# Kernel optimization log

Hardware: AMD Instinct MI355X
Metric: run time of the kernel (lower is better)

Reference implementation:

```python
import jax, jax.numpy as jnp
import numpy as np
from jax import lax

B, FREQ, T = 4, 258, 2176
N_FRAMES, N_SHIFT = 128, 64
W = 32            # number of spectral windows: 128 + 64*k < 2176
H = 5 * 28 * 14   # 1960
NUM_CLASSES = 2


def setup_inputs() -> dict:
    key = jax.random.key(0)
    ks = jax.random.split(key, 13)
    x = jax.random.normal(ks[0], (B, FREQ, T), jnp.float32)
    hx0 = jax.random.normal(ks[1], (B, H), jnp.float32)
    labels = jax.random.randint(ks[2], (B,), 0, NUM_CLASSES, jnp.int64)
    conv1_w = jax.random.normal(ks[3], (64, 1, 9, 9), jnp.float32) * 0.05
    conv1_b = jax.random.normal(ks[4], (64,), jnp.float32) * 0.05
    conv2_w = jax.random.normal(ks[5], (5, 64, 4, 4), jnp.float32) * 0.05
    conv2_b = jax.random.normal(ks[6], (5,), jnp.float32) * 0.05
    w_ih = jax.random.normal(ks[7], (3 * H, H), jnp.float32) * 0.02
    w_hh = jax.random.normal(ks[8], (3 * H, H), jnp.float32) * 0.02
    b_ih = jax.random.normal(ks[9], (3 * H,), jnp.float32) * 0.02
    b_hh = jax.random.normal(ks[10], (3 * H,), jnp.float32) * 0.02
    fc_w = jax.random.normal(ks[11], (NUM_CLASSES, H), jnp.float32) * 0.02
    fc_b = jax.random.normal(ks[12], (NUM_CLASSES,), jnp.float32) * 0.02
    return dict(x=x, hx0=hx0, labels=labels, conv1_w=conv1_w, conv1_b=conv1_b,
                conv2_w=conv2_w, conv2_b=conv2_b, w_ih=w_ih, w_hh=w_hh,
                b_ih=b_ih, b_hh=b_hh, fc_w=fc_w, fc_b=fc_b)


def _conv_sig_pool(y, w, b, pad):
    y = lax.conv_general_dilated(y, w, (1, 1), [(pad, pad), (pad, pad)],
                                 dimension_numbers=('NCHW', 'OIHW', 'NCHW'))
    y = jax.nn.sigmoid(y + b[None, :, None, None])
    return lax.reduce_window(y, -jnp.inf, lax.max, (1, 1, 3, 3), (1, 1, 3, 3), 'VALID')


def reference(x, hx0, labels, conv1_w, conv1_b, conv2_w, conv2_b,
              w_ih, w_hh, b_ih, b_hh, fc_w, fc_b):
    # spectral windows: drop first freq bin, slide window of 128 frames, stride 64
    loc = x[:, 1:, :]                                   # [B, 257, T]
    idx = jnp.arange(W)[:, None] * N_SHIFT + jnp.arange(N_FRAMES)[None, :]
    win = loc[:, :, idx]                                # [B, 257, W, 128]
    win = win.transpose(0, 2, 1, 3).reshape(B * W, 1, 257, N_FRAMES)

    y = _conv_sig_pool(win, conv1_w, conv1_b, 2)        # [B*W, 64, 84, 41]
    y = _conv_sig_pool(y, conv2_w, conv2_b, 2)          # [B*W, 5, 28, 14]
    feat = y.reshape(B, W, H)                           # flatten C,H,W (C-order)

    def gru_step(h, xt):                                # xt: [B, H]
        gi = xt @ w_ih.T + b_ih                         # [B, 3H]
        gh = h @ w_hh.T + b_hh
        i_r, i_z, i_n = jnp.split(gi, 3, axis=1)
        h_r, h_z, h_n = jnp.split(gh, 3, axis=1)
        r = jax.nn.sigmoid(i_r + h_r)
        z = jax.nn.sigmoid(i_z + h_z)
        n = jnp.tanh(i_n + r * h_n)
        return (1.0 - z) * n + z * h, None

    hT, _ = lax.scan(gru_step, hx0, feat.transpose(1, 0, 2))  # scan over W steps

    logits = hT @ fc_w.T + fc_b                         # [B, num_classes]
    samples = jax.nn.softmax(logits, axis=1)
    return (samples, labels)
```

## Files before the change

kernel.cpp:

```cpp
#include <hip/hip_runtime.h>
#include <hip/hip_cooperative_groups.h>

__device__ __forceinline__ float bf2f(unsigned short u) {
  union { unsigned int i; float f; } v; v.i = ((unsigned int)u) << 16; return v.f;
}
__device__ __forceinline__ unsigned short f2bf(float f) {
  union { float f; unsigned int i; } v; v.f = f;
  unsigned int x = v.i;
  return (unsigned short)((x + 0x7fffu + ((x >> 16) & 1u)) >> 16);
}
__device__ __forceinline__ float sigmf(float x) { return 1.f / (1.f + __expf(-x)); }

typedef float f32x4 __attribute__((ext_vector_type(4)));
typedef short short8v __attribute__((ext_vector_type(8)));
typedef short short4v __attribute__((ext_vector_type(4)));

__device__ __forceinline__ short8v pack8(const float* p) {
  union { short8v s; unsigned int u[4]; } r;
#pragma unroll
  for (int i = 0; i < 4; ++i) {
    unsigned int lo = __float_as_uint(p[2 * i]) >> 16;
    unsigned int hi = __float_as_uint(p[2 * i + 1]) & 0xFFFF0000u;
    r.u[i] = hi | lo;
  }
  return r.s;
}

#define KP 1984
#define NP 5888
#define GRU_BLOCKS 245
#define C1_PLANE 2860

__global__ void k_prep(const float* __restrict__ w_hh, unsigned short* __restrict__ whh_bf,
                       const float* __restrict__ w_ih, unsigned short* __restrict__ wih_bf,
                       const float* __restrict__ w1, const float* __restrict__ b1,
                       unsigned short* __restrict__ w1f,
                       const float* __restrict__ w2, unsigned short* __restrict__ w2f,
                       unsigned short* __restrict__ feat_bf,
                       unsigned long long* __restrict__ hb0,
                       unsigned long long* __restrict__ hb1) {
  const int b = blockIdx.x;
  const int tid = threadIdx.x;
  if (b < 2048) {
    const int n4 = 5880 * 1960 / 4;
    for (int i = b * 256 + tid; i < n4; i += 2048 * 256) {
      float4 v = *reinterpret_cast<const float4*>(&w_hh[i * 4]);
      ushort4 u;
      u.x = f2bf(v.x); u.y = f2bf(v.y); u.z = f2bf(v.z); u.w = f2bf(v.w);
      *reinterpret_cast<ushort4*>(&whh_bf[i * 4]) = u;
    }
  } else if (b < 7752) {
    const int total = NP * KP / 8;
    int idx = (b - 2048) * 256 + tid;
    if (idx < total) {
      int row = idx / (KP / 8);
      int c8 = (idx - row * (KP / 8)) * 8;
      short8v v = {0, 0, 0, 0, 0, 0, 0, 0};
      if (row < 5880 && c8 < 1960) {
        const float* s = w_ih + (size_t)row * 1960 + c8;
        if (c8 + 8 <= 1960) {
          float tmp[8];
#pragma unroll
          for (int i = 0; i < 8; ++i) tmp[i] = s[i];
          v = pack8(tmp);
        } else {
          union { short8v s8; unsigned short us[8]; } u; u.s8 = v;
          for (int i = 0; i < 1960 - c8; ++i) u.us[i] = f2bf(s[i]);
          v = u.s8;
        }
      }
      *reinterpret_cast<short8v*>(wih_bf + (size_t)idx * 8) = v;
    }
  } else if (b < 7776) {
    int idx = (b - 7752) * 256 + tid;
    if (idx < 4 * 3 * 64 * 8) {
      int j = idx & 7, l = (idx >> 3) & 63;
      int rest = idx >> 9;
      int s = rest % 3, ocf = rest / 3;
      int oc = ocf * 16 + (l & 15);
      int k = s * 32 + (l >> 4) * 8 + j;
      float v = 0.f;
      if (k < 64)       v = w1[oc * 81 + (k >> 3) * 9 + (k & 7)];
      else if (k < 72)  v = w1[oc * 81 + 72 + (k - 64)];
      else if (k < 80)  v = w1[oc * 81 + (k - 72) * 9 + 8];
      else if (k == 80) v = w1[oc * 81 + 80];
      else if (k == 81) v = b1[oc];
      w1f[idx] = f2bf(v);
    }
  } else if (b < 7840) {
    int idx = (b - 7776) * 256 + tid;
    if (idx < 32 * 64 * 8) {
      int j = idx & 7, l = (idx >> 3) & 63, s = idx >> 9;
      int oc = l & 15;
      int k = s * 32 + (l >> 4) * 8 + j;
      int t = k >> 6, ch = k & 63, fr = t >> 2, fc = t & 3;
      float v = (oc < 5) ? w2[((oc * 64 + ch) * 4 + fr) * 4 + fc] : 0.f;
      w2f[idx] = f2bf(v);
    }
  } else {
    for (int i = tid; i < 128 * 24; i += 256) {
      int n = i / 24, k = 1960 + i % 24;
      feat_bf[(size_t)n * KP + k] = 0;
    }
    for (int i = tid; i < 3920; i += 256) {
      hb0[i] = 0ull;
      hb1[i] = 0ull;
    }
  }
}

__global__ __launch_bounds__(256) void k_conv1(const float* __restrict__ x,
                                               const unsigned short* __restrict__ w1f,
                                               unsigned short* __restrict__ pool1) {
  const int n = blockIdx.x, qrg = blockIdx.y;
  const int b = n >> 5, w = n & 31;
  __shared__ __align__(16) unsigned short s_b[4 * C1_PLANE];
  const int tid = threadIdx.x;
  for (int i = tid; i < 20 * 132; i += 256) {
    int lr = i / 132, lc = i % 132;
    int f = 12 * qrg + lr - 2;
    int t = lc - 2;
    float v = 0.f;
    if (f >= 0 && f < 257 && t >= 0 && t < 128)
      v = x[((size_t)b * 258 + 1 + f) * 2176 + w * 64 + t];
    unsigned short bf = f2bf(v);
#pragma unroll
    for (int m = 0; m < 4; ++m) s_b[m * C1_PLANE + lr * 140 + lc + m] = bf;
  }
  const int lane = tid & 63, wv = tid >> 6;
  short8v bw[4][3];
#pragma unroll
  for (int ocf = 0; ocf < 4; ++ocf)
#pragma unroll
    for (int s = 0; s < 3; ++s)
      bw[ocf][s] = *reinterpret_cast<const short8v*>(&w1f[(((ocf * 3) + s) * 64 + lane) * 8]);
  __syncthreads();

  const int qr = qrg * 4 + wv;
  const int li = lane & 15, g = lane >> 4;

  for (int pgt = 0; pgt < 3; ++pgt) {
    int pg = pgt * 16 + li;
    if (pg > 40) pg = 40;
    f32x4 pm[4];
#pragma unroll
    for (int ocf = 0; ocf < 4; ++ocf) pm[ocf] = (f32x4){-3.4e38f, -3.4e38f, -3.4e38f, -3.4e38f};

    for (int rr = 0; rr < 3; ++rr) {
      const int lrb = 3 * wv + rr;
#pragma unroll
      for (int phi = 0; phi < 3; ++phi) {
        const int c = 3 * pg + phi;
        const int m = (-c) & 3;
        const unsigned short* hb = &s_b[m * C1_PLANE + c + m];
        f32x4 acc[4];
#pragma unroll
        for (int ocf = 0; ocf < 4; ++ocf) acc[ocf] = (f32x4){0.f, 0.f, 0.f, 0.f};
        const unsigned short* p0 = hb + (lrb + g) * 140;
        short8v a0 = __builtin_shufflevector(*reinterpret_cast<const short4v*>(p0),
                                             *reinterpret_cast<const short4v*>(p0 + 4),
                                             0, 1, 2, 3, 4, 5, 6, 7);
#pragma unroll
        for (int ocf = 0; ocf < 4; ++ocf)
          acc[ocf] = __builtin_amdgcn_mfma_f32_16x16x32_bf16(a0, bw[ocf][0], acc[ocf], 0, 0, 0);
        const unsigned short* p1 = p0 + 4 * 140;
        short8v a1 = __builtin_shufflevector(*reinterpret_cast<const short4v*>(p1),
                                             *reinterpret_cast<const short4v*>(p1 + 4),
                                             0, 1, 2, 3, 4, 5, 6, 7);
#pragma unroll
        for (int ocf = 0; ocf < 4; ++ocf)
          acc[ocf] = __builtin_amdgcn_mfma_f32_16x16x32_bf16(a1, bw[ocf][1], acc[ocf], 0, 0, 0);
        short8v a2;
        if (g == 0) {
          const unsigned short* p2 = p0 + 8 * 140;
          a2 = __builtin_shufflevector(*reinterpret_cast<const short4v*>(p2),
                                       *reinterpret_cast<const short4v*>(p2 + 4),
                                       0, 1, 2, 3, 4, 5, 6, 7);
        } else if (g == 1) {
          const unsigned short* pv = &s_b[lrb * 140 + c + 8];
          union { short8v s8; unsigned int u[4]; } r;
          r.u[0] = (unsigned)pv[0]       | ((unsigned)pv[140] << 16);
          r.u[1] = (unsigned)pv[2 * 140] | ((unsigned)pv[3 * 140] << 16);
          r.u[2] = (unsigned)pv[4 * 140] | ((unsigned)pv[5 * 140] << 16);
          r.u[3] = (unsigned)pv[6 * 140] | ((unsigned)pv[7 * 140] << 16);
          a2 = r.s8;
        } else if (g == 2) {
          union { short8v s8; unsigned int u[4]; } r;
          r.u[0] = (unsigned)s_b[(lrb + 8) * 140 + c + 8] | 0x3F800000u;
          r.u[1] = 0; r.u[2] = 0; r.u[3] = 0;
          a2 = r.s8;
        } else {
          a2 = (short8v){0, 0, 0, 0, 0, 0, 0, 0};
        }
#pragma unroll
        for (int ocf = 0; ocf < 4; ++ocf)
          acc[ocf] = __builtin_amdgcn_mfma_f32_16x16x32_bf16(a2, bw[ocf][2], acc[ocf], 0, 0, 0);
#pragma unroll
        for (int ocf = 0; ocf < 4; ++ocf) {
#pragma unroll
          for (int i = 0; i < 4; ++i) pm[ocf][i] = fmaxf(pm[ocf][i], acc[ocf][i]);
        }
      }
    }
#pragma unroll
    for (int ocf = 0; ocf < 4; ++ocf) {
#pragma unroll
      for (int i = 0; i < 4; ++i) {
        int pg2 = pgt * 16 + g * 4 + i;
        if (pg2 <= 40) {
          int oc = ocf * 16 + li;
          pool1[(((size_t)n * 84 + qr) * 41 + pg2) * 64 + oc] = f2bf(sigmf(pm[ocf][i]));
        }
      }
    }
  }
}

__global__ __launch_bounds__(128, 2) void k_conv2(const unsigned short* __restrict__ pool1,
                                                  const unsigned short* __restrict__ w2f,
                                                  const float* __restrict__ b2,
                                                  unsigned short* __restrict__ feat_bf) {
  const int n = blockIdx.x, qg = blockIdx.y;
  __shared__ __align__(16) unsigned short s_a[9 * 46 * 64];
  const int tid = threadIdx.x;
  const int lane = tid & 63, wv = tid >> 6;
  short8v bwr[32];
#pragma unroll
  for (int s = 0; s < 32; ++s)
    bwr[s] = *reinterpret_cast<const short8v*>(&w2f[(s * 64 + lane) * 8]);
  const int r0 = 6 * qg - 2;
  for (int idx = tid; idx < 9 * 46 * 8; idx += 128) {
    int row = idx / (46 * 8);
    int rem = idx - row * (46 * 8);
    int lc = rem >> 3, cp = rem & 7;
    int gr = r0 + row, gc = lc - 2;
    short8v v = {0, 0, 0, 0, 0, 0, 0, 0};
    if ((unsigned)gr < 84u && (unsigned)gc < 41u)
      v = *reinterpret_cast<const short8v*>(&pool1[(((size_t)n * 84 + gr) * 41 + gc) * 64 + cp * 8]);
    int rot = (cp * 8 + lc * 8) & 63;
    *reinterpret_cast<short8v*>(&s_a[(row * 46 + lc) * 64 + rot]) = v;
  }
  __syncthreads();

  const int q = qg * 2 + wv;
  const int li = lane & 15, g = lane >> 4;
  const int pg = li > 13 ? 13 : li;
  f32x4 pm = (f32x4){-3.4e38f, -3.4e38f, -3.4e38f, -3.4e38f};

  for (int rr = 0; rr < 3; ++rr) {
#pragma unroll
    for (int phi = 0; phi < 3; ++phi) {
      f32x4 acc[4];
#pragma unroll
      for (int i = 0; i < 4; ++i) acc[i] = (f32x4){0.f, 0.f, 0.f, 0.f};
#pragma unroll
      for (int s = 0; s < 32; ++s) {
        const int t = s >> 1, h = s & 1;
        const int fr = t >> 2, fc = t & 3;
        const int srow = 3 * wv + rr + fr;
        const int lc = 3 * pg + phi + fc;
        const int rot = (h * 32 + g * 8 + lc * 8) & 63;
        short8v a = *reinterpret_cast<const short8v*>(&s_a[(srow * 46 + lc) * 64 + rot]);
        acc[s & 3] = __builtin_amdgcn_mfma_f32_16x16x32_bf16(a, bwr[s], acc[s & 3], 0, 0, 0);
      }
      f32x4 sum;
#pragma unroll
      for (int i = 0; i < 4; ++i) sum[i] = (acc[0][i] + acc[1][i]) + (acc[2][i] + acc[3][i]);
#pragma unroll
      for (int i = 0; i < 4; ++i) pm[i] = fmaxf(pm[i], sum[i]);
    }
  }
  if (li < 5) {
#pragma unroll
    for (int i = 0; i < 4; ++i) {
      int pq = g * 4 + i;
      if (pq < 14)
        feat_bf[(size_t)n * KP + li * 392 + q * 14 + pq] = f2bf(sigmf(pm[i] + b2[li]));
    }
  }
}

__global__ __launch_bounds__(256) void k_gi(const unsigned short* __restrict__ feat_bf,
                                            const unsigned short* __restrict__ wih_bf,
                                            const float* __restrict__ b_ih,
                                            float* __restrict__ gi) {
  const int bx = blockIdx.x, bm = blockIdx.y;
  const int w = threadIdx.x >> 6, lane = threadIdx.x & 63;
  const int li = lane & 15, g = lane >> 4;
  const unsigned short* ap = feat_bf + (size_t)(bm * 64 + w * 16 + li) * KP + g * 8;
  const unsigned short* bp = wih_bf + (size_t)(bx * 16 + li) * KP + g * 8;
  f32x4 acc0 = (f32x4){0.f, 0.f, 0.f, 0.f};
  f32x4 acc1 = (f32x4){0.f, 0.f, 0.f, 0.f};
  for (int kc = 0; kc < 62; kc += 2) {
    short8v a0 = *reinterpret_cast<const short8v*>(ap + kc * 32);
    short8v b0 = *reinterpret_cast<const short8v*>(bp + kc * 32);
    short8v a1 = *reinterpret_cast<const short8v*>(ap + kc * 32 + 32);
    short8v b1 = *reinterpret_cast<const short8v*>(bp + kc * 32 + 32);
    acc0 = __builtin_amdgcn_mfma_f32_16x16x32_bf16(a0, b0, acc0, 0, 0, 0);
    acc1 = __builtin_amdgcn_mfma_f32_16x16x32_bf16(a1, b1, acc1, 0, 0, 0);
  }
  const int j = bx * 16 + li;
  if (j < 5880) {
    const float bi = b_ih[j];
    const int n0 = bm * 64 + w * 16 + g * 4;
#pragma unroll
    for (int i = 0; i < 4; ++i)
      gi[(size_t)(n0 + i) * 5880 + j] = acc0[i] + acc1[i] + bi;
  }
}

__global__ __launch_bounds__(512) void k_gru(const unsigned short* __restrict__ whh,
                                             const float* __restrict__ b_hh,
                                             const float* __restrict__ gi,
                                             const float* __restrict__ hx0,
                                             unsigned long long* __restrict__ hb0,
                                             unsigned long long* __restrict__ hb1) {
  __shared__ __align__(16) unsigned short s_w[2 * 62 * 64 * 8];
  __shared__ __align__(16) unsigned short s_h[4 * 1984];
  __shared__ float s_part[4 * 2 * 64 * 4];
  __shared__ float s_gi[96];
  const int tid = threadIdx.x;
  const int bid = blockIdx.x;
  const int k0 = bid * 8;
  const int lane = tid & 63, wv = tid >> 6;
  const int li = lane & 15, g2 = lane >> 4;

  for (int idx = tid; idx < 2 * 62 * 64; idx += 512) {
    int mt = idx / 3968;
    int rem = idx - mt * 3968;
    int kc = rem >> 6, l = rem & 63;
    int lli = l & 15, lg2 = l >> 4;
    int k = kc * 32 + lg2 * 8;
    short8v v = {0, 0, 0, 0, 0, 0, 0, 0};
    bool rowok = (mt == 0) ? true : (lli < 8);
    if (rowok && k < 1960) {
      int g = (mt == 0) ? (lli >> 3) : 2;
      int kk = (mt == 0) ? (lli & 7) : lli;
      v = *reinterpret_cast<const short8v*>(&whh[(size_t)(g * 1960 + k0 + kk) * 1960 + k]);
    }
    *reinterpret_cast<short8v*>(&s_w[(size_t)idx * 8]) = v;
  }
  for (int i = tid; i < 4 * 992; i += 512) reinterpret_cast<unsigned int*>(s_h)[i] = 0u;

  float hp0 = 0.f, hp1 = 0.f, bhr0 = 0, bhr1 = 0, bhz0 = 0, bhz1 = 0, bhn0 = 0, bhn1 = 0;
  if (tid < 16) {
    int cb = tid >> 2, p = tid & 3;
    int k = k0 + 2 * p;
    hp0 = hx0[cb * 1960 + k];
    hp1 = hx0[cb * 1960 + k + 1];
    bhr0 = b_hh[k];         bhr1 = b_hh[k + 1];
    bhz0 = b_hh[1960 + k];  bhz1 = b_hh[1960 + k + 1];
    bhn0 = b_hh[3920 + k];  bhn1 = b_hh[3920 + k + 1];
  }
  __syncthreads();

  for (int t = 0; t < 32; ++t) {
    if (t == 0) {
      for (int i = tid; i < 7840; i += 512) {
        int b = i / 1960, k = i - b * 1960;
        s_h[b * 1984 + k] = f2bf(hx0[i]);
      }
    } else {
      const unsigned long long* hin = (t & 1) ? hb1 : hb0;
      unsigned pend = 0;
#pragma unroll
      for (int r = 0; r < 8; ++r)
        if (tid + (r << 9) < 3920) pend |= (1u << r);
      while (pend) {
        unsigned long long v[8];
#pragma unroll
        for (int r = 0; r < 8; ++r)
          if (pend & (1u << r))
            v[r] = __hip_atomic_load(&hin[tid + (r << 9)], __ATOMIC_RELAXED,
                                     __HIP_MEMORY_SCOPE_AGENT);
#pragma unroll
        for (int r = 0; r < 8; ++r) {
          if ((pend & (1u << r)) && (unsigned)(v[r] >> 32) >= (unsigned)t) {
            int i = tid + (r << 9);
            int b = i / 980, kp = i - b * 980;
            reinterpret_cast<unsigned int*>(s_h)[b * 992 + kp] = (unsigned)v[r];
            pend &= ~(1u << r);
          }
        }
        if (pend) __builtin_amdgcn_s_sleep(0);
      }
    }
    if (tid < 96) {
      int gg = tid >> 5, bb = (tid >> 3) & 3, kk = tid & 7;
      s_gi[tid] = gi[(size_t)(bb * 32 + t) * 5880 + gg * 1960 + k0 + kk];
    }
    __syncthreads();

    if (wv < 4) {
      f32x4 acc0 = (f32x4){0.f, 0.f, 0.f, 0.f};
      f32x4 acc1 = (f32x4){0.f, 0.f, 0.f, 0.f};
      for (int kc = wv; kc < 62; kc += 4) {
        short8v bfr = *reinterpret_cast<const short8v*>(&s_h[(li & 3) * 1984 + kc * 32 + g2 * 8]);
        short8v a0 = *reinterpret_cast<const short8v*>(&s_w[((size_t)kc * 64 + lane) * 8]);
        short8v a1 = *reinterpret_cast<const short8v*>(&s_w[((size_t)(62 + kc) * 64 + lane) * 8]);
        acc0 = __builtin_amdgcn_mfma_f32_16x16x32_bf16(a0, bfr, acc0, 0, 0, 0);
        acc1 = __builtin_amdgcn_mfma_f32_16x16x32_bf16(a1, bfr, acc1, 0, 0, 0);
      }
      *reinterpret_cast<f32x4*>(&s_part[((wv * 2 + 0) * 64 + lane) * 4]) = acc0;
      *reinterpret_cast<f32x4*>(&s_part[((wv * 2 + 1) * 64 + lane) * 4]) = acc1;
    }
    __syncthreads();

    unsigned long long* hout = (t & 1) ? hb0 : hb1;
    if (tid < 16) {
      const int cb = tid >> 2, p = tid & 3;
      const int kk = 2 * p;
      auto psum = [&](int mt, int m) -> float {
        int base = mt * 256 + ((m >> 2) * 16 + cb) * 4 + (m & 3);
        return ((s_part[base] + s_part[base + 512]) +
                (s_part[base + 1024] + s_part[base + 1536]));
      };
      float ghr0 = psum(0, kk),     ghr1 = psum(0, kk + 1);
      float ghz0 = psum(0, 8 + kk), ghz1 = psum(0, 8 + kk + 1);
      float ghn0 = psum(1, kk),     ghn1 = psum(1, kk + 1);
      float r0 = sigmf(s_gi[cb * 8 + kk] + ghr0 + bhr0);
      float z0 = sigmf(s_gi[32 + cb * 8 + kk] + ghz0 + bhz0);
      float n0 = tanhf(s_gi[64 + cb * 8 + kk] + r0 * (ghn0 + bhn0));
      float h0v = (1.f - z0) * n0 + z0 * hp0;
      float r1 = sigmf(s_gi[cb * 8 + kk + 1] + ghr1 + bhr1);
      float z1 = sigmf(s_gi[32 + cb * 8 + kk + 1] + ghz1 + bhz1);
      float n1 = tanhf(s_gi[64 + cb * 8 + kk + 1] + r1 * (ghn1 + bhn1));
      float h1v = (1.f - z1) * n1 + z1 * hp1;
      hp0 = h0v; hp1 = h1v;
      unsigned long long packed =
          ((unsigned long long)(unsigned)(t + 1) << 32) |
          (unsigned long long)((unsigned)f2bf(h0v) | ((unsigned)f2bf(h1v) << 16));
      __hip_atomic_store(&hout[cb * 980 + (k0 >> 1) + p], packed,
                         __ATOMIC_RELAXED, __HIP_MEMORY_SCOPE_AGENT);
    }
    __syncthreads();
  }
}

__global__ void k_fc(const unsigned long long* __restrict__ h, const float* __restrict__ fc_w,
                     const float* __restrict__ fc_b, const int* __restrict__ labels,
                     float* __restrict__ out) {
  const int l = threadIdx.x;
  float acc[8];
#pragma unroll
  for (int i = 0; i < 8; ++i) acc[i] = 0.f;
  for (int p = l; p < 980; p += 64) {
    const float w0a = fc_w[2 * p], w0b = fc_w[2 * p + 1];
    const float w1a = fc_w[1960 + 2 * p], w1b = fc_w[1960 + 2 * p + 1];
#pragma unroll
    for (int b = 0; b < 4; ++b) {
      unsigned int d = (unsigned int)h[b * 980 + p];
      float ha = bf2f((unsigned short)(d & 0xffff));
      float hb = bf2f((unsigned short)(d >> 16));
      acc[b * 2 + 0] += ha * w0a + hb * w0b;
      acc[b * 2 + 1] += ha * w1a + hb * w1b;
    }
  }
#pragma unroll
  for (int i = 0; i < 8; ++i) {
    float a = acc[i];
#pragma unroll
    for (int off = 32; off; off >>= 1) a += __shfl_xor(a, off, 64);
    acc[i] = a;
  }
  if (l == 0) {
#pragma unroll
    for (int b = 0; b < 4; ++b) {
      const float l0 = acc[b * 2] + fc_b[0], l1 = acc[b * 2 + 1] + fc_b[1];
      const float m = fmaxf(l0, l1);
      const float e0 = __expf(l0 - m), e1 = __expf(l1 - m);
      const float s = e0 + e1;
      out[b * 2 + 0] = e0 / s;
      out[b * 2 + 1] = e1 / s;
    }
    for (int i = 0; i < 4; ++i) out[8 + i] = (float)labels[i];
  }
}

extern "C" void kernel_launch(void* const* d_in, const int* in_sizes, int n_in,
                              void* d_out, int out_size, void* d_ws, size_t ws_size,
                              hipStream_t stream) {
  const float* x       = (const float*)d_in[0];
  const float* hx0     = (const float*)d_in[1];
  const int*   labels  = (const int*)d_in[2];
  const float* conv1_w = (const float*)d_in[3];
  const float* conv1_b = (const float*)d_in[4];
  const float* conv2_w = (const float*)d_in[5];
  const float* conv2_b = (const float*)d_in[6];
  const float* w_ih    = (const float*)d_in[7];
  const float* w_hh    = (const float*)d_in[8];
  const float* b_ih    = (const float*)d_in[9];
  const float* b_hh    = (const float*)d_in[10];
  const float* fc_w    = (const float*)d_in[11];
  const float* fc_b    = (const float*)d_in[12];

  char* ws = (char*)d_ws;
  size_t off = 0;
  unsigned short* pool1 = (unsigned short*)(ws + off); off += (size_t)128 * 84 * 41 * 64 * 2;
  unsigned short* feat_bf = (unsigned short*)(ws + off); off += (size_t)128 * KP * 2;
  float* gi    = (float*)(ws + off); off += (size_t)128 * 5880 * 4;
  unsigned short* whh_bf = (unsigned short*)(ws + off); off += (size_t)5880 * 1960 * 2;
  unsigned short* wih_bf = (unsigned short*)(ws + off); off += (size_t)NP * KP * 2;
  unsigned long long* hb0 = (unsigned long long*)(ws + off); off += (size_t)4 * 980 * 8;
  unsigned long long* hb1 = (unsigned long long*)(ws + off); off += (size_t)4 * 980 * 8;
  unsigned short* w1f = (unsigned short*)(ws + off); off += (size_t)4 * 3 * 64 * 8 * 2;
  unsigned short* w2f = (unsigned short*)(ws + off); off += (size_t)32 * 64 * 8 * 2;

  k_prep<<<7841, 256, 0, stream>>>(w_hh, whh_bf, w_ih, wih_bf, conv1_w, conv1_b, w1f,
                                   conv2_w, w2f, feat_bf, hb0, hb1);

  dim3 g1(128, 21);
  k_conv1<<<g1, 256, 0, stream>>>(x, w1f, pool1);

  dim3 g2(128, 14);
  k_conv2<<<g2, 128, 0, stream>>>(pool1, w2f, conv2_b, feat_bf);

  dim3 g3(368, 2);
  k_gi<<<g3, 256, 0, stream>>>(feat_bf, wih_bf, b_ih, gi);

  void* gru_args[] = {(void*)&whh_bf, (void*)&b_hh, (void*)&gi, (void*)&hx0,
                      (void*)&hb0, (void*)&hb1};
  hipLaunchCooperativeKernel((const void*)k_gru, dim3(GRU_BLOCKS), dim3(512), gru_args, 0, stream);

  k_fc<<<1, 64, 0, stream>>>(hb0, fc_w, fc_b, labels, (float*)d_out);
}
```

Measured before the change: 389.8 us.

## Convert GRU weights to bf16 inside consumers, fuse FC into GRU kernel

Drops the separate prep pass that converted w_ih and w_hh to bf16 in workspace. k_gi and k_gru now read fp32 weights directly and pack them to bf16 on the fly, which removes a large read, write and reread of about 46M weights. The final FC and softmax move into block 0 of the cooperative GRU kernel, which polls the hidden-state buffer for the final step, so one launch is saved. tanhf is also replaced with an exp-based fast tanh. The cost is doubled global read traffic for the fp32 weight loads in k_gi and the GRU weight staging.

```diff
diff --git a/kernel.cpp b/kernel.cpp
--- a/kernel.cpp
+++ b/kernel.cpp
@@ -10,6 +10,11 @@
   return (unsigned short)((x + 0x7fffu + ((x >> 16) & 1u)) >> 16);
 }
 __device__ __forceinline__ float sigmf(float x) { return 1.f / (1.f + __expf(-x)); }
+__device__ __forceinline__ float tanhfast(float x) {
+  float xc = fminf(fmaxf(x, -15.f), 15.f);
+  float e = __expf(2.f * xc);
+  return (e - 1.f) / (e + 1.f);
+}
 
 typedef float f32x4 __attribute__((ext_vector_type(4)));
 typedef short short8v __attribute__((ext_vector_type(8)));
@@ -31,9 +36,7 @@
 #define GRU_BLOCKS 245
 #define C1_PLANE 2860
 
-__global__ void k_prep(const float* __restrict__ w_hh, unsigned short* __restrict__ whh_bf,
-                       const float* __restrict__ w_ih, unsigned short* __restrict__ wih_bf,
-                       const float* __restrict__ w1, const float* __restrict__ b1,
+__global__ void k_prep(const float* __restrict__ w1, const float* __restrict__ b1,
                        unsigned short* __restrict__ w1f,
                        const float* __restrict__ w2, unsigned short* __restrict__ w2f,
                        unsigned short* __restrict__ feat_bf,
@@ -41,38 +44,8 @@
                        unsigned long long* __restrict__ hb1) {
   const int b = blockIdx.x;
   const int tid = threadIdx.x;
-  if (b < 2048) {
-    const int n4 = 5880 * 1960 / 4;
-    for (int i = b * 256 + tid; i < n4; i += 2048 * 256) {
-      float4 v = *reinterpret_cast<const float4*>(&w_hh[i * 4]);
-      ushort4 u;
-      u.x = f2bf(v.x); u.y = f2bf(v.y); u.z = f2bf(v.z); u.w = f2bf(v.w);
-      *reinterpret_cast<ushort4*>(&whh_bf[i * 4]) = u;
-    }
-  } else if (b < 7752) {
-    const int total = NP * KP / 8;
-    int idx = (b - 2048) * 256 + tid;
-    if (idx < total) {
-      int row = idx / (KP / 8);
-      int c8 = (idx - row * (KP / 8)) * 8;
-      short8v v = {0, 0, 0, 0, 0, 0, 0, 0};
-      if (row < 5880 && c8 < 1960) {
-        const float* s = w_ih + (size_t)row * 1960 + c8;
-        if (c8 + 8 <= 1960) {
-          float tmp[8];
-#pragma unroll
-          for (int i = 0; i < 8; ++i) tmp[i] = s[i];
-          v = pack8(tmp);
-        } else {
-          union { short8v s8; unsigned short us[8]; } u; u.s8 = v;
-          for (int i = 0; i < 1960 - c8; ++i) u.us[i] = f2bf(s[i]);
-          v = u.s8;
-        }
-      }
-      *reinterpret_cast<short8v*>(wih_bf + (size_t)idx * 8) = v;
-    }
-  } else if (b < 7776) {
-    int idx = (b - 7752) * 256 + tid;
+  if (b < 24) {
+    int idx = b * 256 + tid;
     if (idx < 4 * 3 * 64 * 8) {
       int j = idx & 7, l = (idx >> 3) & 63;
       int rest = idx >> 9;
@@ -87,8 +60,8 @@
       else if (k == 81) v = b1[oc];
       w1f[idx] = f2bf(v);
     }
-  } else if (b < 7840) {
-    int idx = (b - 7776) * 256 + tid;
+  } else if (b < 88) {
+    int idx = (b - 24) * 256 + tid;
     if (idx < 32 * 64 * 8) {
       int j = idx & 7, l = (idx >> 3) & 63, s = idx >> 9;
       int oc = l & 15;
@@ -281,25 +254,27 @@
 }
 
 __global__ __launch_bounds__(256) void k_gi(const unsigned short* __restrict__ feat_bf,
-                                            const unsigned short* __restrict__ wih_bf,
+                                            const float* __restrict__ w_ih,
                                             const float* __restrict__ b_ih,
                                             float* __restrict__ gi) {
   const int bx = blockIdx.x, bm = blockIdx.y;
   const int w = threadIdx.x >> 6, lane = threadIdx.x & 63;
   const int li = lane & 15, g = lane >> 4;
+  const int j = bx * 16 + li;
+  const int jc = j < 5880 ? j : 5879;
   const unsigned short* ap = feat_bf + (size_t)(bm * 64 + w * 16 + li) * KP + g * 8;
-  const unsigned short* bp = wih_bf + (size_t)(bx * 16 + li) * KP + g * 8;
+  const float* bp = w_ih + (size_t)jc * 1960 + g * 8;
+  const short8v z8 = {0, 0, 0, 0, 0, 0, 0, 0};
   f32x4 acc0 = (f32x4){0.f, 0.f, 0.f, 0.f};
   f32x4 acc1 = (f32x4){0.f, 0.f, 0.f, 0.f};
   for (int kc = 0; kc < 62; kc += 2) {
     short8v a0 = *reinterpret_cast<const short8v*>(ap + kc * 32);
-    short8v b0 = *reinterpret_cast<const short8v*>(bp + kc * 32);
     short8v a1 = *reinterpret_cast<const short8v*>(ap + kc * 32 + 32);
-    short8v b1 = *reinterpret_cast<const short8v*>(bp + kc * 32 + 32);
+    short8v b0 = pack8(bp + kc * 32);
+    short8v b1 = (kc != 60 || g == 0) ? pack8(bp + kc * 32 + 32) : z8;
     acc0 = __builtin_amdgcn_mfma_f32_16x16x32_bf16(a0, b0, acc0, 0, 0, 0);
     acc1 = __builtin_amdgcn_mfma_f32_16x16x32_bf16(a1, b1, acc1, 0, 0, 0);
   }
-  const int j = bx * 16 + li;
   if (j < 5880) {
     const float bi = b_ih[j];
     const int n0 = bm * 64 + w * 16 + g * 4;
@@ -309,12 +284,16 @@
   }
 }
 
-__global__ __launch_bounds__(512) void k_gru(const unsigned short* __restrict__ whh,
+__global__ __launch_bounds__(512) void k_gru(const float* __restrict__ whh,
                                              const float* __restrict__ b_hh,
                                              const float* __restrict__ gi,
                                              const float* __restrict__ hx0,
                                              unsigned long long* __restrict__ hb0,
-                                             unsigned long long* __restrict__ hb1) {
+                                             unsigned long long* __restrict__ hb1,
+                                             const float* __restrict__ fc_w,
+                                             const float* __restrict__ fc_b,
+                                             const int* __restrict__ labels,
+                                             float* __restrict__ out) {
   __shared__ __align__(16) unsigned short s_w[2 * 62 * 64 * 8];
   __shared__ __align__(16) unsigned short s_h[4 * 1984];
   __shared__ float s_part[4 * 2 * 64 * 4];
@@ -336,7 +315,7 @@
     if (rowok && k < 1960) {
       int g = (mt == 0) ? (lli >> 3) : 2;
       int kk = (mt == 0) ? (lli & 7) : lli;
-      v = *reinterpret_cast<const short8v*>(&whh[(size_t)(g * 1960 + k0 + kk) * 1960 + k]);
+      v = pack8(&whh[(size_t)(g * 1960 + k0 + kk) * 1960 + k]);
     }
     *reinterpret_cast<short8v*>(&s_w[(size_t)idx * 8]) = v;
   }
@@ -420,11 +399,11 @@
       float ghn0 = psum(1, kk),     ghn1 = psum(1, kk + 1);
       float r0 = sigmf(s_gi[cb * 8 + kk] + ghr0 + bhr0);
       float z0 = sigmf(s_gi[32 + cb * 8 + kk] + ghz0 + bhz0);
-      float n0 = tanhf(s_gi[64 + cb * 8 + kk] + r0 * (ghn0 + bhn0));
+      float n0 = tanhfast(s_gi[64 + cb * 8 + kk] + r0 * (ghn0 + bhn0));
       float h0v = (1.f - z0) * n0 + z0 * hp0;
       float r1 = sigmf(s_gi[cb * 8 + kk + 1] + ghr1 + bhr1);
       float z1 = sigmf(s_gi[32 + cb * 8 + kk + 1] + ghz1 + bhz1);
-      float n1 = tanhf(s_gi[64 + cb * 8 + kk + 1] + r1 * (ghn1 + bhn1));
+      float n1 = tanhfast(s_gi[64 + cb * 8 + kk + 1] + r1 * (ghn1 + bhn1));
       float h1v = (1.f - z1) * n1 + z1 * hp1;
       hp0 = h0v; hp1 = h1v;
       unsigned long long packed =
@@ -435,45 +414,65 @@
     }
     __syncthreads();
   }
-}
-
-__global__ void k_fc(const unsigned long long* __restrict__ h, const float* __restrict__ fc_w,
-                     const float* __restrict__ fc_b, const int* __restrict__ labels,
-                     float* __restrict__ out) {
-  const int l = threadIdx.x;
-  float acc[8];
-#pragma unroll
-  for (int i = 0; i < 8; ++i) acc[i] = 0.f;
-  for (int p = l; p < 980; p += 64) {
-    const float w0a = fc_w[2 * p], w0b = fc_w[2 * p + 1];
-    const float w1a = fc_w[1960 + 2 * p], w1b = fc_w[1960 + 2 * p + 1];
-#pragma unroll
-    for (int b = 0; b < 4; ++b) {
-      unsigned int d = (unsigned int)h[b * 980 + p];
-      float ha = bf2f((unsigned short)(d & 0xffff));
-      float hb = bf2f((unsigned short)(d >> 16));
-      acc[b * 2 + 0] += ha * w0a + hb * w0b;
-      acc[b * 2 + 1] += ha * w1a + hb * w1b;
-    }
-  }
-#pragma unroll
-  for (int i = 0; i < 8; ++i) {
-    float a = acc[i];
-#pragma unroll
-    for (int off = 32; off; off >>= 1) a += __shfl_xor(a, off, 64);
-    acc[i] = a;
-  }
-  if (l == 0) {
-#pragma unroll
-    for (int b = 0; b < 4; ++b) {
-      const float l0 = acc[b * 2] + fc_b[0], l1 = acc[b * 2 + 1] + fc_b[1];
-      const float m = fmaxf(l0, l1);
-      const float e0 = __expf(l0 - m), e1 = __expf(l1 - m);
-      const float s = e0 + e1;
-      out[b * 2 + 0] = e0 / s;
-      out[b * 2 + 1] = e1 / s;
-    }
-    for (int i = 0; i < 4; ++i) out[8 + i] = (float)labels[i];
+
+  if (bid == 0) {
+    unsigned pend = 0;
+#pragma unroll
+    for (int r = 0; r < 8; ++r)
+      if (tid + (r << 9) < 3920) pend |= (1u << r);
+    while (pend) {
+      unsigned long long v[8];
+#pragma unroll
+      for (int r = 0; r < 8; ++r)
+        if (pend & (1u << r))
+          v[r] = __hip_atomic_load(&hb0[tid + (r << 9)], __ATOMIC_RELAXED,
+                                   __HIP_MEMORY_SCOPE_AGENT);
+#pragma unroll
+      for (int r = 0; r < 8; ++r) {
+        if ((pend & (1u << r)) && (unsigned)(v[r] >> 32) >= 32u) {
+          int i = tid + (r << 9);
+          int b = i / 980, kp = i - b * 980;
+          reinterpret_cast<unsigned int*>(s_h)[b * 992 + kp] = (unsigned)v[r];
+          pend &= ~(1u << r);
+        }
+      }
+      if (pend) __builtin_amdgcn_s_sleep(0);
+    }
+    __syncthreads();
+    if (tid < 64) {
+      const int l = tid;
+      float acc[8];
+#pragma unroll
+      for (int i = 0; i < 8; ++i) acc[i] = 0.f;
+      for (int k = l; k < 1960; k += 64) {
+        const float w0 = fc_w[k], w1 = fc_w[1960 + k];
+#pragma unroll
+        for (int b = 0; b < 4; ++b) {
+          const float hv = bf2f(s_h[b * 1984 + k]);
+          acc[b * 2 + 0] += hv * w0;
+          acc[b * 2 + 1] += hv * w1;
+        }
+      }
+#pragma unroll
+      for (int i = 0; i < 8; ++i) {
+        float a = acc[i];
+#pragma unroll
+        for (int off = 32; off; off >>= 1) a += __shfl_xor(a, off, 64);
+        acc[i] = a;
+      }
+      if (l == 0) {
+#pragma unroll
+        for (int b = 0; b < 4; ++b) {
+          const float l0 = acc[b * 2] + fc_b[0], l1 = acc[b * 2 + 1] + fc_b[1];
+          const float m = fmaxf(l0, l1);
+          const float e0 = __expf(l0 - m), e1 = __expf(l1 - m);
+          const float s = e0 + e1;
+          out[b * 2 + 0] = e0 / s;
+          out[b * 2 + 1] = e1 / s;
+        }
+        for (int i = 0; i < 4; ++i) out[8 + i] = (float)labels[i];
+      }
+    }
   }
 }
 
@@ -499,15 +498,12 @@
   unsigned short* pool1 = (unsigned short*)(ws + off); off += (size_t)128 * 84 * 41 * 64 * 2;
   unsigned short* feat_bf = (unsigned short*)(ws + off); off += (size_t)128 * KP * 2;
   float* gi    = (float*)(ws + off); off += (size_t)128 * 5880 * 4;
-  unsigned short* whh_bf = (unsigned short*)(ws + off); off += (size_t)5880 * 1960 * 2;
-  unsigned short* wih_bf = (unsigned short*)(ws + off); off += (size_t)NP * KP * 2;
   unsigned long long* hb0 = (unsigned long long*)(ws + off); off += (size_t)4 * 980 * 8;
   unsigned long long* hb1 = (unsigned long long*)(ws + off); off += (size_t)4 * 980 * 8;
   unsigned short* w1f = (unsigned short*)(ws + off); off += (size_t)4 * 3 * 64 * 8 * 2;
   unsigned short* w2f = (unsigned short*)(ws + off); off += (size_t)32 * 64 * 8 * 2;
 
-  k_prep<<<7841, 256, 0, stream>>>(w_hh, whh_bf, w_ih, wih_bf, conv1_w, conv1_b, w1f,
-                                   conv2_w, w2f, feat_bf, hb0, hb1);
+  k_prep<<<89, 256, 0, stream>>>(conv1_w, conv1_b, w1f, conv2_w, w2f, feat_bf, hb0, hb1);
 
   dim3 g1(128, 21);
   k_conv1<<<g1, 256, 0, stream>>>(x, w1f, pool1);
@@ -516,11 +512,10 @@
   k_conv2<<<g2, 128, 0, stream>>>(pool1, w2f, conv2_b, feat_bf);
 
   dim3 g3(368, 2);
-  k_gi<<<g3, 256, 0, stream>>>(feat_bf, wih_bf, b_ih, gi);
-
-  void* gru_args[] = {(void*)&whh_bf, (void*)&b_hh, (void*)&gi, (void*)&hx0,
-                      (void*)&hb0, (void*)&hb1};
+  k_gi<<<g3, 256, 0, stream>>>(feat_bf, w_ih, b_ih, gi);
+
+  void* gru_args[] = {(void*)&w_hh, (void*)&b_hh, (void*)&gi, (void*)&hx0,
+                      (void*)&hb0, (void*)&hb1, (void*)&fc_w, (void*)&fc_b,
+                      (void*)&labels, (void*)&d_out};
   hipLaunchCooperativeKernel((const void*)k_gru, dim3(GRU_BLOCKS), dim3(512), gru_args, 0, stream);
-
-  k_fc<<<1, 64, 0, stream>>>(hb0, fc_w, fc_b, labels, (float*)d_out);
-}
+}
```

New measurement: 372.4 us. -4.5%, faster.
